# Performance work log

Measured on AMD Instinct MI355X. Metric: run time of the kernel, lower is better.

## Reference

```python
import jax, jax.numpy as jnp
import numpy as np


def _l2norm(x, axis):
    # F.normalize: x / max(||x||_2, eps)
    n = jnp.sqrt(jnp.sum(x * x, axis=axis, keepdims=True))
    return x / jnp.maximum(n, 1e-12)


def setup_inputs() -> dict:
    key = jax.random.key(0)
    k1, k2 = jax.random.split(key)
    B, N, H = 32768, 2048, 512
    z = jax.random.normal(k1, (B, H), dtype=jnp.float32)
    memory_items = jax.random.normal(k2, (N, H), dtype=jnp.float32)
    return {"z": z, "memory_items": memory_items}


def reference(z, memory_items):
    # ---- read path: cosine-similarity attention over memory bank ----
    z_n = _l2norm(z, axis=1)                     # (B,H)
    m_n = _l2norm(memory_items, axis=1)          # (N,H)
    similarity = z_n @ m_n.T                     # (B,N)
    weights = jax.nn.softmax(similarity, axis=1)  # (B,N)
    z_hat = weights @ memory_items               # (B,H)

    # ---- update path (no-grad in original): vectorized over slots ----
    # row b is "relevant" to slot i iff weights[b,i] >= max_j weights[b,j]
    # (slot i is an argmax for row b). Per-slot softmax over the relevant
    # rows' similarity column, then weighted sum of z -> scatter-add.
    maxw = jnp.max(weights, axis=1, keepdims=True)   # (B,1)
    mask = weights >= maxw                            # (B,N) bool
    neg = jnp.finfo(similarity.dtype).min
    s = jnp.where(mask, similarity, neg)              # (B,N)
    m = jnp.max(s, axis=0)                            # (N,) column max
    p = jnp.where(mask, jnp.exp(s - m), 0.0)          # (B,N)
    denom = jnp.sum(p, axis=0)                        # (N,)
    u = p / jnp.maximum(denom, 1e-30)                 # (B,N) masked softmax per column
    update_term = u.T @ z                             # (N,H)
    count = jnp.sum(mask, axis=0)                     # (N,)
    new_memory = jnp.where(
        (count > 0)[:, None],
        _l2norm(memory_items + update_term, axis=1),
        memory_items,
    )
    return z_hat, new_memory
```

## Files before the change

kernel.cpp:

```cpp
#include <hip/hip_runtime.h>
#include <math.h>

#define B_ROWS 32768
#define N_SLOTS 2048
#define H_DIM 512
#define MCAP 4096

typedef __attribute__((ext_vector_type(8))) _Float16 f16x8;
typedef __attribute__((ext_vector_type(4))) float f32x4;

#define ZPL 132
#define FIX_MARGIN 2.5e-4f
#define XROWS 16

__device__ __forceinline__ unsigned short f2h(float f) {
    union { _Float16 h; unsigned short u; } cv;
    cv.h = (_Float16)f;
    return cv.u;
}
__device__ __forceinline__ unsigned pk2h(float a, float b) {
    return (unsigned)f2h(a) | ((unsigned)f2h(b) << 16);
}
__device__ __forceinline__ unsigned fenc(float f) {
    unsigned b = __float_as_uint(f);
    return (b & 0x80000000u) ? ~b : (b | 0x80000000u);
}

#define STAGE16(g, l) __builtin_amdgcn_global_load_lds( \
    (const __attribute__((address_space(1))) unsigned int*)(g), \
    (__attribute__((address_space(3))) unsigned int*)(l), 16, 0, 0)

#define VWAIT4() asm volatile("s_waitcnt vmcnt(4)" ::: "memory")
#define LWAIT0() asm volatile("s_waitcnt lgkmcnt(0)" ::: "memory")


__global__ __launch_bounds__(256) void prep_z_k(const float* __restrict__ z,
                                                float* __restrict__ zinv) {
    int row = blockIdx.x * 4 + (threadIdx.x >> 6);
    int lane = threadIdx.x & 63;
    const float4* p = reinterpret_cast<const float4*>(z + (size_t)row * H_DIM);
    float4 a = p[lane * 2];
    float4 b = p[lane * 2 + 1];
    float s = a.x * a.x + a.y * a.y + a.z * a.z + a.w * a.w
            + b.x * b.x + b.y * b.y + b.z * b.z + b.w * b.w;
#pragma unroll
    for (int m = 32; m >= 1; m >>= 1) s += __shfl_xor(s, m, 64);
    if (lane == 0) zinv[row] = 1.0f / fmaxf(sqrtf(s), 1e-12f);
}

__global__ __launch_bounds__(256) void prep_mem_k(const float* __restrict__ mem,
                                                  float* __restrict__ minv,
                                                  short* __restrict__ mn_sw) {
    int row = blockIdx.x * 4 + (threadIdx.x >> 6);
    int lane = threadIdx.x & 63;
    const float4* p = reinterpret_cast<const float4*>(mem + (size_t)row * H_DIM);
    float4 a = p[lane * 2];
    float4 b = p[lane * 2 + 1];
    float s = a.x * a.x + a.y * a.y + a.z * a.z + a.w * a.w
            + b.x * b.x + b.y * b.y + b.z * b.z + b.w * b.w;
#pragma unroll
    for (int m = 32; m >= 1; m >>= 1) s += __shfl_xor(s, m, 64);
    float inv = 1.0f / fmaxf(sqrtf(s), 1e-12f);
    if (lane == 0) minv[row] = inv;
    uint4 w;
    w.x = pk2h(a.x * inv, a.y * inv);
    w.y = pk2h(a.z * inv, a.w * inv);
    w.z = pk2h(b.x * inv, b.y * inv);
    w.w = pk2h(b.z * inv, b.w * inv);
    char* dst = (char*)mn_sw + ((size_t)row << 10) + ((unsigned)(lane * 16) ^ (unsigned)((row & 7) << 4));
    *reinterpret_cast<uint4*>(dst) = w;
}

__global__ __launch_bounds__(256) void prep_memT_k(const float* __restrict__ mem,
                                                   short* __restrict__ memT_sw) {
    __shared__ short Ts[64][72];
    int bs = blockIdx.x;
    int bh = blockIdx.y;
    int tid = threadIdx.x;
    {
        int s = tid >> 2, c4 = (tid & 3) * 16;
        const float* src = mem + (size_t)(bs * 64 + s) * H_DIM + bh * 64 + c4;
#pragma unroll
        for (int j = 0; j < 4; ++j) {
            float4 v = *reinterpret_cast<const float4*>(src + j * 4);
            Ts[s][c4 + j * 4 + 0] = (short)f2h(v.x);
            Ts[s][c4 + j * 4 + 1] = (short)f2h(v.y);
            Ts[s][c4 + j * 4 + 2] = (short)f2h(v.z);
            Ts[s][c4 + j * 4 + 3] = (short)f2h(v.w);
        }
    }
    __syncthreads();
    int h = tid >> 2, q = tid & 3;
    unsigned w[8];
#pragma unroll
    for (int k = 0; k < 8; ++k) {
        unsigned lo = (unsigned short)Ts[q * 16 + 2 * k][h];
        unsigned hi = (unsigned short)Ts[q * 16 + 2 * k + 1][h];
        w[k] = lo | (hi << 16);
    }
    uint4 c0 = {w[0], w[1], w[2], w[3]};
    uint4 c1 = {w[4], w[5], w[6], w[7]};
    char* dst = (char*)memT_sw + (size_t)(bh * 64 + h) * (N_SLOTS * 2);
    unsigned sw = (unsigned)((h & 7) << 4);
    unsigned b0 = (unsigned)(bs * 128 + q * 32);
    *reinterpret_cast<uint4*>(dst + (b0 ^ sw)) = c0;
    *reinterpret_cast<uint4*>(dst + ((b0 + 16) ^ sw)) = c1;
}


__global__ __launch_bounds__(512, 2) void zhat_k(const float* __restrict__ z,
                                                 const short* __restrict__ mn_sw,
                                                 const short* __restrict__ memT_sw,
                                                 const float* __restrict__ zinv,
                                                 float* __restrict__ rowmax,
                                                 int* __restrict__ rowarg,
                                                 float* __restrict__ rowm2,
                                                 float* __restrict__ out) {
    __shared__ __align__(16) short Mb[4][8192];
    __shared__ __align__(16) short Pl[64 * ZPL];
    __shared__ float pm1[2][64], pm2[2][64], ps[2][64];
    __shared__ int pa1[2][64], pa2[2][64];

    int tid = threadIdx.x;
    int row0 = blockIdx.x * 64;
    int wave = tid >> 6, lane = tid & 63;
    int lm = lane & 15, quad = lane >> 4;
    int rt = wave & 3;
    int wg = wave >> 2;
    const int swz = (lm & 7) << 4;

#define STAGE_M(buf, c0, kc) do { \
        const char* _g = (const char*)mn_sw + ((size_t)((c0) + wave * 16 + (lane >> 3)) << 10) \
                         + ((kc) << 7) + ((lane & 7) << 4); \
        short* _l = &Mb[buf][wave * 16 * 64]; \
        STAGE16(_g, _l); \
        STAGE16(_g + (8 << 10), _l + 8 * 64); \
    } while (0)

#define STAGE_V(buf, c0, hc) do { \
        const char* _g = (const char*)memT_sw + ((size_t)((hc) * 64 + wave * 8 + (lane >> 4)) << 12) \
                         + ((size_t)(c0) << 1) + ((lane & 15) << 4); \
        short* _l = &Mb[buf][wave * 8 * 128]; \
        STAGE16(_g, _l); \
        STAGE16(_g + (4 << 12), _l + 4 * 128); \
    } while (0)

    STAGE_M(0, 0, 0);
    STAGE_M(1, 0, 1);

    int zrow = row0 + rt * 16 + lm;
    float zi = zinv[zrow];
    f16x8 Zfr[16];
#pragma unroll
    for (int kt = 0; kt < 16; ++kt) {
        const float* zp = z + (size_t)zrow * H_DIM + kt * 32 + quad * 8;
        float4 a = *reinterpret_cast<const float4*>(zp);
        float4 b = *reinterpret_cast<const float4*>(zp + 4);
        union { uint4 u; f16x8 v; } cv;
        cv.u.x = pk2h(a.x * zi, a.y * zi);
        cv.u.y = pk2h(a.z * zi, a.w * zi);
        cv.u.z = pk2h(b.x * zi, b.y * zi);
        cv.u.w = pk2h(b.z * zi, b.w * zi);
        Zfr[kt] = cv.v;
    }

    f32x4 acc[16];
#pragma unroll
    for (int t = 0; t < 16; ++t) acc[t] = (f32x4){0.f, 0.f, 0.f, 0.f};
    float rm1[4], rm2[4], lsum[4];
    int ra1[4], ra2[4];
#pragma unroll
    for (int r = 0; r < 4; ++r) {
        rm1[r] = -3.4e38f; rm2[r] = -3.4e38f; lsum[r] = 0.f; ra1[r] = 0; ra2[r] = 0;
    }

    for (int ct = 0; ct < 16; ++ct) {
        int col0 = ct * 128;
        int col0n = (ct < 15) ? col0 + 128 : 0;
        f32x4 sacc[4];
#pragma unroll
        for (int i = 0; i < 4; ++i) sacc[i] = (f32x4){0.f, 0.f, 0.f, 0.f};

#pragma unroll
        for (int kc = 0; kc < 8; ++kc) {
            if (kc < 6)       STAGE_M((kc + 2) & 3, col0, kc + 2);
            else if (kc == 6) STAGE_V(0, col0, 0);
            else              STAGE_V(1, col0, 1);
            VWAIT4();
            __builtin_amdgcn_s_barrier();
            __builtin_amdgcn_s_setprio(1);
#pragma unroll
            for (int ks = 0; ks < 2; ++ks) {
                f16x8 af = Zfr[kc * 2 + ks];
#pragma unroll
                for (int i = 0; i < 4; ++i) {
                    int srow = (wg * 4 + i) * 16 + lm;
                    int kb = (ks * 64 + quad * 16) ^ swz;
                    f16x8 bfr = *reinterpret_cast<const f16x8*>(
                        (const char*)&Mb[kc & 3][0] + srow * 128 + kb);
                    sacc[i] = __builtin_amdgcn_mfma_f32_16x16x32_f16(af, bfr, sacc[i], 0, 0, 0);
                }
            }
            __builtin_amdgcn_s_setprio(0);
        }

#pragma unroll
        for (int i = 0; i < 4; ++i) {
            int sl = (wg * 4 + i) * 16 + lm;
            int sg = col0 + sl;
#pragma unroll
            for (int r = 0; r < 4; ++r) {
                float v = sacc[i][r];
                if (v > rm1[r]) { rm2[r] = rm1[r]; ra2[r] = ra1[r]; rm1[r] = v; ra1[r] = sg; }
                else if (v > rm2[r]) { rm2[r] = v; ra2[r] = sg; }
                float p = __expf(v);
                lsum[r] += p;
                Pl[(rt * 16 + quad * 4 + r) * ZPL + sl] = (short)f2h(p);
            }
        }
        LWAIT0();
        __builtin_amdgcn_s_barrier();

        f16x8 pa[4];
#pragma unroll
        for (int ks = 0; ks < 4; ++ks)
            pa[ks] = *reinterpret_cast<const f16x8*>(&Pl[(rt * 16 + lm) * ZPL + ks * 32 + quad * 8]);

#pragma unroll
        for (int hc = 0; hc < 8; ++hc) {
            if (hc < 6)       STAGE_V((hc + 2) & 3, col0, hc + 2);
            else if (hc == 6) STAGE_M(0, col0n, 0);
            else              STAGE_M(1, col0n, 1);
            VWAIT4();
            __builtin_amdgcn_s_barrier();
            __builtin_amdgcn_s_setprio(1);
#pragma unroll
            for (int ks = 0; ks < 4; ++ks) {
#pragma unroll
                for (int i = 0; i < 2; ++i) {
                    int hl = (wg * 2 + i) * 16 + lm;
                    int kb = (ks * 64 + quad * 16) ^ swz;
                    f16x8 bfr = *reinterpret_cast<const f16x8*>(
                        (const char*)&Mb[hc & 3][0] + hl * 256 + kb);
                    acc[hc * 2 + i] = __builtin_amdgcn_mfma_f32_16x16x32_f16(pa[ks], bfr, acc[hc * 2 + i], 0, 0, 0);
                }
            }
            __builtin_amdgcn_s_setprio(0);
        }
    }
    __syncthreads();

#pragma unroll
    for (int mk = 1; mk < 16; mk <<= 1) {
#pragma unroll
        for (int r = 0; r < 4; ++r) {
            float n1 = __shfl_xor(rm1[r], mk, 16);
            int b1 = __shfl_xor(ra1[r], mk, 16);
            float n2 = __shfl_xor(rm2[r], mk, 16);
            int b2 = __shfl_xor(ra2[r], mk, 16);
            if (n1 > rm1[r]) {
                bool c = rm1[r] > n2;
                rm2[r] = c ? rm1[r] : n2; ra2[r] = c ? ra1[r] : b2;
                rm1[r] = n1; ra1[r] = b1;
            } else {
                bool c = n1 > rm2[r];
                rm2[r] = c ? n1 : rm2[r]; ra2[r] = c ? b1 : ra2[r];
            }
            lsum[r] += __shfl_xor(lsum[r], mk, 16);
        }
    }
    if (lm == 0) {
#pragma unroll
        for (int r = 0; r < 4; ++r) {
            int rl = rt * 16 + quad * 4 + r;
            pm1[wg][rl] = rm1[r]; pa1[wg][rl] = ra1[r];
            pm2[wg][rl] = rm2[r]; pa2[wg][rl] = ra2[r];
            ps[wg][rl] = lsum[r];
        }
    }
    __syncthreads();
    if (wave == 0) {
        int r = lane;
        float gm1 = pm1[0][r], gm2 = pm2[0][r];
        int ga1 = pa1[0][r], ga2 = pa2[0][r];
        float n1 = pm1[1][r]; int b1 = pa1[1][r];
        float n2 = pm2[1][r]; int b2 = pa2[1][r];
        if (n1 > gm1) {
            bool c = gm1 > n2;
            gm2 = c ? gm1 : n2; ga2 = c ? ga1 : b2;
            gm1 = n1; ga1 = b1;
        } else {
            bool c = n1 > gm2;
            gm2 = c ? n1 : gm2; ga2 = c ? b1 : ga2;
        }
        rowmax[row0 + r] = gm1; rowarg[row0 + r] = ga1; rowm2[row0 + r] = gm2;
    }
    float linv[4];
#pragma unroll
    for (int r = 0; r < 4; ++r) {
        int rl = rt * 16 + quad * 4 + r;
        linv[r] = 1.0f / (ps[0][rl] + ps[1][rl]);
    }
#pragma unroll
    for (int hc = 0; hc < 8; ++hc)
#pragma unroll
        for (int i = 0; i < 2; ++i) {
            int t = hc * 2 + i;
            int h = hc * 64 + (wg * 2 + i) * 16 + lm;
#pragma unroll
            for (int r = 0; r < 4; ++r) {
                int rg = row0 + rt * 16 + quad * 4 + r;
                out[(size_t)rg * H_DIM + h] = acc[t][r] * linv[r];
            }
        }
}


__global__ void zero_k(int* __restrict__ cnt) {
    if (threadIdx.x == 0) *cnt = 0;
}

__global__ __launch_bounds__(256) void flag_k(const float* __restrict__ rowmax,
                                              const float* __restrict__ rowm2,
                                              int* __restrict__ cnt,
                                              int* __restrict__ list,
                                              unsigned long long* __restrict__ packed) {
    int b = blockIdx.x * 256 + threadIdx.x;
    if (rowmax[b] - rowm2[b] < FIX_MARGIN) {
        int p = atomicAdd(cnt, 1);
        list[p] = b;
        packed[p] = 0ull;
    }
}


__global__ __launch_bounds__(256) void exact_k(const float* __restrict__ z,
                                               const float* __restrict__ mem,
                                               const float* __restrict__ minv,
                                               const int* __restrict__ cnt,
                                               const int* __restrict__ list,
                                               unsigned long long* __restrict__ packed) {
    __shared__ float As[32][XROWS + 4];
    __shared__ float Bs[32][132];
    __shared__ int rows[XROWS];
    int tid = threadIdx.x;
    int tx = tid & 15, ty = tid >> 4;
    int n = *cnt;
    int ngroups = (n + XROWS - 1) / XROWS;
    int nunits = ngroups * 16;

    for (int u = blockIdx.x; u < nunits; u += gridDim.x) {
        int g = u >> 4;
        int col0 = (u & 15) * 128;
        __syncthreads();
        if (tid < XROWS) {
            int idx = g * XROWS + tid;
            rows[tid] = list[idx < n ? idx : n - 1];
        }
        __syncthreads();
        float acc[8];
#pragma unroll
        for (int j = 0; j < 8; ++j) acc[j] = 0.f;
        for (int kc = 0; kc < H_DIM; kc += 32) {
            if (tid < 128) {
                int r = tid >> 3, k4 = (tid & 7) * 4;
                float4 v = *reinterpret_cast<const float4*>(z + (size_t)rows[r] * H_DIM + kc + k4);
                As[k4 + 0][r] = v.x;
                As[k4 + 1][r] = v.y;
                As[k4 + 2][r] = v.z;
                As[k4 + 3][r] = v.w;
            }
            int sl = tid >> 1, kq = (tid & 1) * 16;
#pragma unroll
            for (int j = 0; j < 4; ++j) {
                float4 v = *reinterpret_cast<const float4*>(mem + (size_t)(col0 + sl) * H_DIM + kc + kq + j * 4);
                Bs[kq + j * 4 + 0][sl] = v.x;
                Bs[kq + j * 4 + 1][sl] = v.y;
                Bs[kq + j * 4 + 2][sl] = v.z;
                Bs[kq + j * 4 + 3][sl] = v.w;
            }
            __syncthreads();
#pragma unroll 4
            for (int k = 0; k < 32; ++k) {
                float av = As[k][ty];
                const float4 b0 = *reinterpret_cast<const float4*>(&Bs[k][tx * 8]);
                const float4 b1 = *reinterpret_cast<const float4*>(&Bs[k][tx * 8 + 4]);
                acc[0] = fmaf(av, b0.x, acc[0]);
                acc[1] = fmaf(av, b0.y, acc[1]);
                acc[2] = fmaf(av, b0.z, acc[2]);
                acc[3] = fmaf(av, b0.w, acc[3]);
                acc[4] = fmaf(av, b1.x, acc[4]);
                acc[5] = fmaf(av, b1.y, acc[5]);
                acc[6] = fmaf(av, b1.z, acc[6]);
                acc[7] = fmaf(av, b1.w, acc[7]);
            }
            __syncthreads();
        }
        float runM = -3.4e38f;
        int runA = 0;
#pragma unroll
        for (int j = 0; j < 8; ++j) {
            int sg = col0 + tx * 8 + j;
            float s = acc[j] * minv[sg];
            if (s > runM) { runM = s; runA = sg; }
        }
#pragma unroll
        for (int mk = 1; mk < 16; mk <<= 1) {
            float om = __shfl_xor(runM, mk, 16);
            int oa = __shfl_xor(runA, mk, 16);
            if (om > runM || (om == runM && oa < runA)) { runM = om; runA = oa; }
        }
        if (tx == 0) {
            int idx = g * XROWS + ty;
            int tgt = idx < n ? idx : n - 1;
            unsigned long long pk =
                ((unsigned long long)fenc(runM) << 32) | (unsigned)(2047 - runA);
            atomicMax(&packed[tgt], pk);
        }
    }
}

__global__ __launch_bounds__(256) void unpack_k(const int* __restrict__ cnt,
                                                const int* __restrict__ list,
                                                const unsigned long long* __restrict__ packed,
                                                int* __restrict__ rowarg) {
    int p = blockIdx.x * 256 + threadIdx.x;
    if (p < *cnt) {
        int slot = 2047 - (int)(unsigned)(packed[p] & 0xFFFFFFFFull);
        rowarg[list[p]] = slot;
    }
}


__global__ __launch_bounds__(256) void refine_k(const float* __restrict__ z,
                                                const float* __restrict__ mem,
                                                const float* __restrict__ zinv,
                                                const float* __restrict__ minv,
                                                const int* __restrict__ rowarg,
                                                float* __restrict__ rowmax) {
    int row = blockIdx.x * 4 + (threadIdx.x >> 6);
    int lane = threadIdx.x & 63;
    int a = rowarg[row];
    const float4* zp = reinterpret_cast<const float4*>(z + (size_t)row * H_DIM);
    const float4* mp = reinterpret_cast<const float4*>(mem + (size_t)a * H_DIM);
    float d = 0.f;
#pragma unroll
    for (int j = 0; j < 2; ++j) {
        float4 x = zp[lane + j * 64];
        float4 y = mp[lane + j * 64];
        d += x.x * y.x + x.y * y.y + x.z * y.z + x.w * y.w;
    }
#pragma unroll
    for (int m = 32; m >= 1; m >>= 1) d += __shfl_xor(d, m, 64);
    if (lane == 0) rowmax[row] = d * zinv[row] * minv[a];
}


__global__ __launch_bounds__(256) void slot_update_k(const float* __restrict__ mem,
                                                     const float* __restrict__ z,
                                                     const float* __restrict__ rowmax,
                                                     const int* __restrict__ rowarg,
                                                     float* __restrict__ outmem) {
    __shared__ int members[MCAP];
    __shared__ float uval[MCAP];
    __shared__ int cnt;
    __shared__ float red[4];
    __shared__ float bcast;
    int slot = blockIdx.x, tid = threadIdx.x;
    if (tid == 0) cnt = 0;
    __syncthreads();
    for (int b = tid; b < B_ROWS; b += 256) {
        if (rowarg[b] == slot) {
            int p = atomicAdd(&cnt, 1);
            if (p < MCAP) members[p] = b;
        }
    }
    __syncthreads();
    int n = min(cnt, MCAP);
    size_t base = (size_t)slot * H_DIM;
    if (n == 0) {
        for (int h = tid; h < H_DIM; h += 256) outmem[base + h] = mem[base + h];
        return;
    }
    float lm = -3.4e38f;
    for (int j = tid; j < n; j += 256) lm = fmaxf(lm, rowmax[members[j]]);
#pragma unroll
    for (int m = 32; m >= 1; m >>= 1) lm = fmaxf(lm, __shfl_xor(lm, m, 64));
    if ((tid & 63) == 0) red[tid >> 6] = lm;
    __syncthreads();
    if (tid == 0) bcast = fmaxf(fmaxf(red[0], red[1]), fmaxf(red[2], red[3]));
    __syncthreads();
    float mslot = bcast;
    __syncthreads();
    float ls = 0.f;
    for (int j = tid; j < n; j += 256) {
        float u = expf(rowmax[members[j]] - mslot);
        uval[j] = u;
        ls += u;
    }
#pragma unroll
    for (int m = 32; m >= 1; m >>= 1) ls += __shfl_xor(ls, m, 64);
    if ((tid & 63) == 0) red[tid >> 6] = ls;
    __syncthreads();
    if (tid == 0) bcast = (red[0] + red[1]) + (red[2] + red[3]);
    __syncthreads();
    float dinv = 1.0f / fmaxf(bcast, 1e-30f);
    float v0 = mem[base + tid];
    float v1 = mem[base + 256 + tid];
    for (int j = 0; j < n; ++j) {
        float u = uval[j] * dinv;
        size_t zb = (size_t)members[j] * H_DIM;
        v0 = fmaf(u, z[zb + tid], v0);
        v1 = fmaf(u, z[zb + 256 + tid], v1);
    }
    float s = v0 * v0 + v1 * v1;
#pragma unroll
    for (int m = 32; m >= 1; m >>= 1) s += __shfl_xor(s, m, 64);
    if ((tid & 63) == 0) red[tid >> 6] = s;
    __syncthreads();
    if (tid == 0) bcast = (red[0] + red[1]) + (red[2] + red[3]);
    __syncthreads();
    float ninv = 1.0f / fmaxf(sqrtf(bcast), 1e-12f);
    outmem[base + tid] = v0 * ninv;
    outmem[base + 256 + tid] = v1 * ninv;
}


extern "C" void kernel_launch(void* const* d_in, const int* in_sizes, int n_in,
                              void* d_out, int out_size, void* d_ws, size_t ws_size,
                              hipStream_t stream) {
    const float* z = (const float*)d_in[0];
    const float* mem = (const float*)d_in[1];
    float* out_zhat = (float*)d_out;
    float* out_mem = out_zhat + (size_t)B_ROWS * H_DIM;

    char* ws = (char*)d_ws;
    size_t off = 0;
    auto alloc = [&](size_t bytes) -> void* {
        void* p = ws + off;
        off += (bytes + 255) & ~(size_t)255;
        return p;
    };
    float* rowmax = (float*)alloc((size_t)B_ROWS * 4);
    int* rowarg = (int*)alloc((size_t)B_ROWS * 4);
    float* rowm2 = (float*)alloc((size_t)B_ROWS * 4);
    float* zinv = (float*)alloc((size_t)B_ROWS * 4);
    float* minv = (float*)alloc((size_t)N_SLOTS * 4);
    short* mn_sw = (short*)alloc((size_t)N_SLOTS * H_DIM * 2);
    short* memT_sw = (short*)alloc((size_t)H_DIM * N_SLOTS * 2);
    int* fcnt = (int*)alloc(256);
    int* flist = (int*)alloc((size_t)B_ROWS * 4);
    unsigned long long* packed = (unsigned long long*)alloc((size_t)B_ROWS * 8);

    prep_z_k<<<B_ROWS / 4, 256, 0, stream>>>(z, zinv);
    prep_mem_k<<<N_SLOTS / 4, 256, 0, stream>>>(mem, minv, mn_sw);
    prep_memT_k<<<dim3(N_SLOTS / 64, H_DIM / 64), 256, 0, stream>>>(mem, memT_sw);
    zhat_k<<<B_ROWS / 64, 512, 0, stream>>>(z, mn_sw, memT_sw, zinv,
                                            rowmax, rowarg, rowm2, out_zhat);
    zero_k<<<1, 64, 0, stream>>>(fcnt);
    flag_k<<<B_ROWS / 256, 256, 0, stream>>>(rowmax, rowm2, fcnt, flist, packed);
    exact_k<<<2048, 256, 0, stream>>>(z, mem, minv, fcnt, flist, packed);
    unpack_k<<<B_ROWS / 256, 256, 0, stream>>>(fcnt, flist, packed, rowarg);
    refine_k<<<B_ROWS / 4, 256, 0, stream>>>(z, mem, zinv, minv, rowarg, rowmax);
    slot_update_k<<<N_SLOTS, 256, 0, stream>>>(mem, z, rowmax, rowarg, out_mem);
}
```

Before: 547.0 us.

## Read V operand directly from global memory in zhat PV GEMM, drop LDS staging

The P·V stage of zhat_k no longer stages the transposed fp16 memory into LDS through the async pipeline. Each wave now loads its V fragments straight from an unswizzled global memT buffer, which the L2 is expected to serve, and computes a 32-row by 128-column output tile instead of the old 16x128 split. Because the PV loop no longer uses the LDS buffers, the QK loop can prefetch the next column tile's M chunks earlier. The zero_k launch is folded into prep_z_k to save one kernel launch. The risk is extra global and L2 traffic and exposed load latency in the MFMA loop, since those loads no longer go through the software pipeline.

```diff
diff --git a/kernel.cpp b/kernel.cpp
--- a/kernel.cpp
+++ b/kernel.cpp
@@ -35,7 +35,9 @@
 
 
 __global__ __launch_bounds__(256) void prep_z_k(const float* __restrict__ z,
-                                                float* __restrict__ zinv) {
+                                                float* __restrict__ zinv,
+                                                int* __restrict__ fcnt) {
+    if (blockIdx.x == 0 && threadIdx.x == 0) *fcnt = 0;
     int row = blockIdx.x * 4 + (threadIdx.x >> 6);
     int lane = threadIdx.x & 63;
     const float4* p = reinterpret_cast<const float4*>(z + (size_t)row * H_DIM);
@@ -72,7 +74,7 @@
 }
 
 __global__ __launch_bounds__(256) void prep_memT_k(const float* __restrict__ mem,
-                                                   short* __restrict__ memT_sw) {
+                                                   short* __restrict__ memT) {
     __shared__ short Ts[64][72];
     int bs = blockIdx.x;
     int bh = blockIdx.y;
@@ -100,17 +102,16 @@
     }
     uint4 c0 = {w[0], w[1], w[2], w[3]};
     uint4 c1 = {w[4], w[5], w[6], w[7]};
-    char* dst = (char*)memT_sw + (size_t)(bh * 64 + h) * (N_SLOTS * 2);
-    unsigned sw = (unsigned)((h & 7) << 4);
+    char* dst = (char*)memT + (size_t)(bh * 64 + h) * (N_SLOTS * 2);
     unsigned b0 = (unsigned)(bs * 128 + q * 32);
-    *reinterpret_cast<uint4*>(dst + (b0 ^ sw)) = c0;
-    *reinterpret_cast<uint4*>(dst + ((b0 + 16) ^ sw)) = c1;
+    *reinterpret_cast<uint4*>(dst + b0) = c0;
+    *reinterpret_cast<uint4*>(dst + b0 + 16) = c1;
 }
 
 
 __global__ __launch_bounds__(512, 2) void zhat_k(const float* __restrict__ z,
                                                  const short* __restrict__ mn_sw,
-                                                 const short* __restrict__ memT_sw,
+                                                 const short* __restrict__ memT,
                                                  const float* __restrict__ zinv,
                                                  float* __restrict__ rowmax,
                                                  int* __restrict__ rowarg,
@@ -127,6 +128,8 @@
     int lm = lane & 15, quad = lane >> 4;
     int rt = wave & 3;
     int wg = wave >> 2;
+    int rh = wave & 1;
+    int wc = wave >> 1;
     const int swz = (lm & 7) << 4;
 
 #define STAGE_M(buf, c0, kc) do { \
@@ -135,14 +138,6 @@
         short* _l = &Mb[buf][wave * 16 * 64]; \
         STAGE16(_g, _l); \
         STAGE16(_g + (8 << 10), _l + 8 * 64); \
-    } while (0)
-
-#define STAGE_V(buf, c0, hc) do { \
-        const char* _g = (const char*)memT_sw + ((size_t)((hc) * 64 + wave * 8 + (lane >> 4)) << 12) \
-                         + ((size_t)(c0) << 1) + ((lane & 15) << 4); \
-        short* _l = &Mb[buf][wave * 8 * 128]; \
-        STAGE16(_g, _l); \
-        STAGE16(_g + (4 << 12), _l + 4 * 128); \
     } while (0)
 
     STAGE_M(0, 0, 0);
@@ -183,9 +178,8 @@
 
 #pragma unroll
         for (int kc = 0; kc < 8; ++kc) {
-            if (kc < 6)       STAGE_M((kc + 2) & 3, col0, kc + 2);
-            else if (kc == 6) STAGE_V(0, col0, 0);
-            else              STAGE_V(1, col0, 1);
+            if (kc < 6) STAGE_M((kc + 2) & 3, col0, kc + 2);
+            else        STAGE_M((kc + 2) & 3, col0n, kc - 6);
             VWAIT4();
             __builtin_amdgcn_s_barrier();
             __builtin_amdgcn_s_setprio(1);
@@ -221,31 +215,21 @@
         LWAIT0();
         __builtin_amdgcn_s_barrier();
 
-        f16x8 pa[4];
-#pragma unroll
-        for (int ks = 0; ks < 4; ++ks)
-            pa[ks] = *reinterpret_cast<const f16x8*>(&Pl[(rt * 16 + lm) * ZPL + ks * 32 + quad * 8]);
-
-#pragma unroll
-        for (int hc = 0; hc < 8; ++hc) {
-            if (hc < 6)       STAGE_V((hc + 2) & 3, col0, hc + 2);
-            else if (hc == 6) STAGE_M(0, col0n, 0);
-            else              STAGE_M(1, col0n, 1);
-            VWAIT4();
-            __builtin_amdgcn_s_barrier();
-            __builtin_amdgcn_s_setprio(1);
-#pragma unroll
-            for (int ks = 0; ks < 4; ++ks) {
-#pragma unroll
-                for (int i = 0; i < 2; ++i) {
-                    int hl = (wg * 2 + i) * 16 + lm;
-                    int kb = (ks * 64 + quad * 16) ^ swz;
-                    f16x8 bfr = *reinterpret_cast<const f16x8*>(
-                        (const char*)&Mb[hc & 3][0] + hl * 256 + kb);
-                    acc[hc * 2 + i] = __builtin_amdgcn_mfma_f32_16x16x32_f16(pa[ks], bfr, acc[hc * 2 + i], 0, 0, 0);
-                }
-            }
-            __builtin_amdgcn_s_setprio(0);
+        const char* vb = (const char*)memT
+            + ((size_t)(wc * 128 + lm) * N_SLOTS + col0 + quad * 8) * 2;
+#pragma unroll
+        for (int ks = 0; ks < 4; ++ks) {
+            f16x8 pa0 = *reinterpret_cast<const f16x8*>(
+                &Pl[((rh * 2 + 0) * 16 + lm) * ZPL + ks * 32 + quad * 8]);
+            f16x8 pa1 = *reinterpret_cast<const f16x8*>(
+                &Pl[((rh * 2 + 1) * 16 + lm) * ZPL + ks * 32 + quad * 8]);
+#pragma unroll
+            for (int hsub = 0; hsub < 8; ++hsub) {
+                f16x8 vf = *reinterpret_cast<const f16x8*>(
+                    vb + (size_t)hsub * 16 * (N_SLOTS * 2) + ks * 64);
+                acc[hsub * 2 + 0] = __builtin_amdgcn_mfma_f32_16x16x32_f16(pa0, vf, acc[hsub * 2 + 0], 0, 0, 0);
+                acc[hsub * 2 + 1] = __builtin_amdgcn_mfma_f32_16x16x32_f16(pa1, vf, acc[hsub * 2 + 1], 0, 0, 0);
+            }
         }
     }
     __syncthreads();
@@ -295,30 +279,28 @@
         }
         rowmax[row0 + r] = gm1; rowarg[row0 + r] = ga1; rowm2[row0 + r] = gm2;
     }
-    float linv[4];
-#pragma unroll
-    for (int r = 0; r < 4; ++r) {
-        int rl = rt * 16 + quad * 4 + r;
-        linv[r] = 1.0f / (ps[0][rl] + ps[1][rl]);
-    }
-#pragma unroll
-    for (int hc = 0; hc < 8; ++hc)
-#pragma unroll
-        for (int i = 0; i < 2; ++i) {
-            int t = hc * 2 + i;
-            int h = hc * 64 + (wg * 2 + i) * 16 + lm;
+    float linv2[2][4];
+#pragma unroll
+    for (int rtl = 0; rtl < 2; ++rtl)
+#pragma unroll
+        for (int r = 0; r < 4; ++r) {
+            int rl = (rh * 2 + rtl) * 16 + quad * 4 + r;
+            linv2[rtl][r] = 1.0f / (ps[0][rl] + ps[1][rl]);
+        }
+#pragma unroll
+    for (int hsub = 0; hsub < 8; ++hsub)
+#pragma unroll
+        for (int rtl = 0; rtl < 2; ++rtl) {
+            int t = hsub * 2 + rtl;
+            int h = wc * 128 + hsub * 16 + lm;
 #pragma unroll
             for (int r = 0; r < 4; ++r) {
-                int rg = row0 + rt * 16 + quad * 4 + r;
-                out[(size_t)rg * H_DIM + h] = acc[t][r] * linv[r];
-            }
-        }
-}
-
-
-__global__ void zero_k(int* __restrict__ cnt) {
-    if (threadIdx.x == 0) *cnt = 0;
-}
+                int rg = row0 + (rh * 2 + rtl) * 16 + quad * 4 + r;
+                out[(size_t)rg * H_DIM + h] = acc[t][r] * linv2[rtl][r];
+            }
+        }
+}
+
 
 __global__ __launch_bounds__(256) void flag_k(const float* __restrict__ rowmax,
                                               const float* __restrict__ rowm2,
@@ -547,17 +529,16 @@
     float* zinv = (float*)alloc((size_t)B_ROWS * 4);
     float* minv = (float*)alloc((size_t)N_SLOTS * 4);
     short* mn_sw = (short*)alloc((size_t)N_SLOTS * H_DIM * 2);
-    short* memT_sw = (short*)alloc((size_t)H_DIM * N_SLOTS * 2);
+    short* memT = (short*)alloc((size_t)H_DIM * N_SLOTS * 2);
     int* fcnt = (int*)alloc(256);
     int* flist = (int*)alloc((size_t)B_ROWS * 4);
     unsigned long long* packed = (unsigned long long*)alloc((size_t)B_ROWS * 8);
 
-    prep_z_k<<<B_ROWS / 4, 256, 0, stream>>>(z, zinv);
+    prep_z_k<<<B_ROWS / 4, 256, 0, stream>>>(z, zinv, fcnt);
     prep_mem_k<<<N_SLOTS / 4, 256, 0, stream>>>(mem, minv, mn_sw);
-    prep_memT_k<<<dim3(N_SLOTS / 64, H_DIM / 64), 256, 0, stream>>>(mem, memT_sw);
-    zhat_k<<<B_ROWS / 64, 512, 0, stream>>>(z, mn_sw, memT_sw, zinv,
+    prep_memT_k<<<dim3(N_SLOTS / 64, H_DIM / 64), 256, 0, stream>>>(mem, memT);
+    zhat_k<<<B_ROWS / 64, 512, 0, stream>>>(z, mn_sw, memT, zinv,
                                             rowmax, rowarg, rowm2, out_zhat);
-    zero_k<<<1, 64, 0, stream>>>(fcnt);
     flag_k<<<B_ROWS / 256, 256, 0, stream>>>(rowmax, rowm2, fcnt, flist, packed);
     exact_k<<<2048, 256, 0, stream>>>(z, mem, minv, fcnt, flist, packed);
     unpack_k<<<B_ROWS / 256, 256, 0, stream>>>(fcnt, flist, packed, rowarg);
```

Result: slower. 692.0 us (+26.5%).
